# Performance work log

Hardware: AMD Instinct MI355X
Metric: run time of the kernel (lower is better)

## Reference

```python
import math
import jax, jax.numpy as jnp
import numpy as np

K_MODES = 8
L_ITERS = 8
ALPHA_INIT = 2000.0
TAU_INIT = 0.01


def setup_inputs() -> dict:
    key = jax.random.key(0)
    B, T, C = 64, 4096, 16
    x = jax.random.normal(key, (B, T, C), dtype=jnp.float32)
    log_alpha = jnp.full((L_ITERS, K_MODES), math.log(ALPHA_INIT), dtype=jnp.float32)
    raw_tau = jnp.full((L_ITERS,), math.log(math.expm1(TAU_INIT) + 1e-08), dtype=jnp.float32)
    omega_init = np.linspace(0.05, 0.45, K_MODES)
    raw_omega = jnp.asarray(np.log(2.0 * omega_init / (1.0 - 2.0 * omega_init + 1e-08)), dtype=jnp.float32)
    return {"x": x, "log_alpha": log_alpha, "raw_tau": raw_tau, "raw_omega": raw_omega}


def reference(x, log_alpha, raw_tau, raw_omega):
    B, T, C = x.shape
    L, K = log_alpha.shape
    T_rfft = T // 2 + 1

    alpha = jnp.exp(log_alpha)                    # (L, K)
    tau = jax.nn.softplus(raw_tau)                # (L,)
    omega = jax.nn.sigmoid(raw_omega) * 0.5       # (K,)

    freqs = jnp.linspace(0.0, 0.5, T_rfft, dtype=x.dtype)  # (T_rfft,)
    # (B, T, C) -> (B*C, T)
    x_bc = jnp.transpose(x, (0, 2, 1)).reshape(B * C, T)
    f_hat = jnp.fft.rfft(x_bc, axis=-1)           # (B*C, T_rfft) complex

    # Precompute all denominators: (L, K, T_rfft)
    denom = 1.0 + 2.0 * alpha[:, :, None] * (freqs[None, None, :] - omega[None, :, None]) ** 2

    u0 = jnp.zeros((B * C, K, T_rfft), dtype=f_hat.dtype)
    lam0 = jnp.zeros_like(f_hat)

    def step(carry, per_layer):
        u, lam = carry
        den_l, tau_l = per_layer
        u_sum = u.sum(axis=1)  # (B*C, T_rfft)
        # Jacobi update for all K modes simultaneously
        numerator = f_hat[:, None, :] - (u_sum[:, None, :] - u) + 0.5 * lam[:, None, :]
        u_new = numerator / den_l[None, :, :]
        lam_new = lam + tau_l * (f_hat - u_new.sum(axis=1))
        return (u_new, lam_new), None

    (u_final, _), _ = jax.lax.scan(step, (u0, lam0), (denom, tau))

    modes_flat = jnp.fft.irfft(u_final, n=T, axis=-1)  # (B*C, K, T)
    modes = jnp.transpose(modes_flat.reshape(B, C, K, T), (0, 2, 3, 1))  # (B, K, T, C)
    return modes
```

## Files before the change

kernel.cpp:

```cpp
#include <hip/hip_runtime.h>
#include <math.h>

#ifndef M_PI
#define M_PI 3.14159265358979323846
#endif

#define T_LEN 4096
#define M_LEN 2048
#define NFREQ 2049
#define KM 8
#define LI 8
#define CD 16

#define SWZ(i) ((i) ^ (((i) >> 4) & 15))

template <int NT>
__device__ __forceinline__ float2* fft2048(float2* a, float2* b, int tid, float sign) {
    float2* src = a;
    float2* dst = b;
    int l = 1024;
    #pragma unroll 1
    for (int s = 0; s < 11; ++s) {
        float piol = sign * (float)M_PI / (float)l;
        #pragma unroll
        for (int ii = 0; ii < 1024 / NT; ++ii) {
            int i = tid + ii * NT;
            int j = i >> s;
            float2 A = src[i];
            float2 B = src[i + 1024];
            float ang = piol * (float)j;
            float sw, cw;
            __sincosf(ang, &sw, &cw);
            float2 sum = make_float2(A.x + B.x, A.y + B.y);
            float2 dif = make_float2(A.x - B.x, A.y - B.y);
            float2 tw = make_float2(dif.x * cw - dif.y * sw, dif.x * sw + dif.y * cw);
            int p = i + (j << s);
            dst[p] = sum;
            dst[p + (1 << s)] = tw;
        }
        __syncthreads();
        float2* t = src; src = dst; dst = t;
        l >>= 1;
    }
    return src;
}

__global__ void __launch_bounds__(512)
k_fwd_iter(const float* __restrict__ x,
           const float* __restrict__ log_alpha,
           const float* __restrict__ raw_tau,
           const float* __restrict__ raw_omega,
           float2* __restrict__ u_ws)
{
    __shared__ float2 bufA[M_LEN];
    __shared__ float2 bufB[M_LEN];
    __shared__ float s_2a[LI * KM];
    __shared__ float s_tau2[LI];
    __shared__ float s_om[KM];

    const int tid = threadIdx.x;
    const int row = blockIdx.x;
    const int b = row >> 4;
    const int c = row & 15;

    if (tid < LI * KM) s_2a[tid]   = 2.0f * __expf(log_alpha[tid]);
    if (tid < LI)      s_tau2[tid] = 0.5f * log1pf(__expf(raw_tau[tid]));
    if (tid < KM)      s_om[tid]   = 0.5f / (1.0f + __expf(-raw_omega[tid]));

    const float* xr = x + (size_t)b * T_LEN * CD + c;
    #pragma unroll
    for (int q = 0; q < 4; ++q) {
        int n = tid + q * 512;
        float e = xr[(size_t)(2 * n) * CD];
        float o = xr[(size_t)(2 * n + 1) * CD];
        bufA[n] = make_float2(e, o);
    }
    __syncthreads();

    float2* Z = fft2048<512>(bufA, bufB, tid, -1.0f);

    const size_t sb = (size_t)(b * (KM * CD) + c);

    for (int f = tid; f < NFREQ; f += 512) {
        float2 Zk = Z[f & (M_LEN - 1)];
        float2 Zm = Z[(M_LEN - f) & (M_LEN - 1)];
        float2 E = make_float2(0.5f * (Zk.x + Zm.x), 0.5f * (Zk.y - Zm.y));
        float2 D = make_float2(0.5f * (Zk.x - Zm.x), 0.5f * (Zk.y + Zm.y));
        float2 O = make_float2(D.y, -D.x);
        float ang = -2.0f * (float)M_PI * (float)f / (float)T_LEN;
        float sw, cw;
        __sincosf(ang, &sw, &cw);
        float fhx = E.x + cw * O.x - sw * O.y;
        float fhy = E.y + cw * O.y + sw * O.x;

        float freq = (float)f * (0.5f / (float)M_LEN);
        float dd[KM];
        #pragma unroll
        for (int k = 0; k < KM; ++k) {
            float d = freq - s_om[k];
            dd[k] = d * d;
        }

        float2 u[KM];
        float sx, sy;
        float hx, hy;

        {
            float nsx = 0.f, nsy = 0.f;
            #pragma unroll
            for (int k = 0; k < KM; ++k) {
                float den = fmaf(s_2a[k], dd[k], 1.0f);
                float r = __builtin_amdgcn_rcpf(den);
                float ux = fhx * r;
                float uy = fhy * r;
                u[k].x = ux; u[k].y = uy;
                nsx += ux; nsy += uy;
            }
            hx = s_tau2[0] * (fhx - nsx);
            hy = s_tau2[0] * (fhy - nsy);
            sx = nsx; sy = nsy;
        }

        #pragma unroll
        for (int l = 1; l < LI; ++l) {
            float bx = fhx - sx + hx;
            float by = fhy - sy + hy;
            float nsx = 0.f, nsy = 0.f;
            #pragma unroll
            for (int k = 0; k < KM; ++k) {
                float den = fmaf(s_2a[l * KM + k], dd[k], 1.0f);
                float r = __builtin_amdgcn_rcpf(den);
                float ux = (bx + u[k].x) * r;
                float uy = (by + u[k].y) * r;
                u[k].x = ux; u[k].y = uy;
                nsx += ux; nsy += uy;
            }
            hx += s_tau2[l] * (fhx - nsx);
            hy += s_tau2[l] * (fhy - nsy);
            sx = nsx; sy = nsy;
        }

        #pragma unroll
        for (int k = 0; k < KM; ++k) {
            u_ws[(sb + (size_t)k * CD) * NFREQ + f] = u[k];
        }
    }
}

#define R2STAGE(S, SRC, DST, CW, SN) {                                        \
    int j_ = tid >> (S);                                                      \
    float2 A_ = SRC[SWZ(tid)];                                                \
    float2 B_ = SRC[SWZ(tid + 1024)];                                         \
    float2 sum_ = make_float2(A_.x + B_.x, A_.y + B_.y);                      \
    float2 dif_ = make_float2(A_.x - B_.x, A_.y - B_.y);                      \
    float2 tw_ = make_float2(dif_.x * (CW) - dif_.y * (SN),                   \
                             dif_.x * (SN) + dif_.y * (CW));                  \
    int p_ = tid + (j_ << (S));                                               \
    DST[SWZ(p_)] = sum_;                                                      \
    DST[SWZ(p_ + (1 << (S)))] = tw_;                                          \
    __syncthreads();                                                          \
}

#define R2STAGE9(SRC, DST) {                                                  \
    float2 A_ = SRC[SWZ(tid)];                                                \
    float2 B_ = SRC[SWZ(tid + 1024)];                                         \
    float2 sum_ = make_float2(A_.x + B_.x, A_.y + B_.y);                      \
    float2 dif_ = make_float2(A_.x - B_.x, A_.y - B_.y);                      \
    float2 tw_ = (tid & 512) ? make_float2(-dif_.y, dif_.x) : dif_;           \
    int p_ = tid + ((tid >> 9) << 9);                                         \
    DST[SWZ(p_)] = sum_;                                                      \
    DST[SWZ(p_ + 512)] = tw_;                                                 \
    __syncthreads();                                                          \
}

#define R2STAGE10(SRC, DST) {                                                 \
    float2 A_ = SRC[SWZ(tid)];                                                \
    float2 B_ = SRC[SWZ(tid + 1024)];                                         \
    DST[SWZ(tid)] = make_float2(A_.x + B_.x, A_.y + B_.y);                    \
    DST[SWZ(tid + 1024)] = make_float2(A_.x - B_.x, A_.y - B_.y);             \
    __syncthreads();                                                          \
}

__global__ void __launch_bounds__(1024)
k_inv(const float2* __restrict__ u_ws, float* __restrict__ out)
{
    __shared__ float2 bufA[NFREQ];
    __shared__ float2 bufB[M_LEN];
    const int tid = threadIdx.x;
    const int bk = blockIdx.x;

    float cs0,sn0,cs1,sn1,cs2,sn2,cs3,sn3,cs4,sn4,cs5,sn5,cs6,sn6,cs7,sn7,cs8,sn8;
    {
        const float w = (float)M_PI / 1024.0f;
        __sincosf(w * (float)tid,          &sn0, &cs0);
        __sincosf(w * (float)(tid & ~1),   &sn1, &cs1);
        __sincosf(w * (float)(tid & ~3),   &sn2, &cs2);
        __sincosf(w * (float)(tid & ~7),   &sn3, &cs3);
        __sincosf(w * (float)(tid & ~15),  &sn4, &cs4);
        __sincosf(w * (float)(tid & ~31),  &sn5, &cs5);
        __sincosf(w * (float)(tid & ~63),  &sn6, &cs6);
        __sincosf(w * (float)(tid & ~127), &sn7, &cs7);
        __sincosf(w * (float)(tid & ~255), &sn8, &cs8);
    }
    float csR, snR;
    __sincosf(((float)M_PI / 2048.0f) * (float)tid, &snR, &csR);

    float val[CD][4];

    #pragma unroll
    for (int c = 0; c < CD; ++c) {
        const float2* sp = u_ws + (size_t)(bk * CD + c) * NFREQ;
        bufA[SWZ(tid)] = sp[tid];
        bufA[SWZ(tid + 1024)] = sp[tid + 1024];
        if (tid == 0) bufA[2048] = sp[2048];
        __syncthreads();

        const float sc = 1.0f / (float)M_LEN;
        #pragma unroll
        for (int jj = 0; jj < 2; ++jj) {
            int j = tid + jj * 1024;
            float cw = jj ? -snR : csR;
            float sw = jj ?  csR : snR;
            float2 Xj = bufA[SWZ(j)];
            float2 Xm = (j > 0) ? bufA[SWZ(M_LEN - j)] : bufA[2048];
            float2 E = make_float2(0.5f * (Xj.x + Xm.x), 0.5f * (Xj.y - Xm.y));
            float2 D = make_float2(0.5f * (Xj.x - Xm.x), 0.5f * (Xj.y + Xm.y));
            float2 O = make_float2(cw * D.x - sw * D.y, cw * D.y + sw * D.x);
            bufB[SWZ(j)] = make_float2((E.x - O.y) * sc, (E.y + O.x) * sc);
        }
        __syncthreads();

        R2STAGE(0, bufB, bufA, cs0, sn0);
        R2STAGE(1, bufA, bufB, cs1, sn1);
        R2STAGE(2, bufB, bufA, cs2, sn2);
        R2STAGE(3, bufA, bufB, cs3, sn3);
        R2STAGE(4, bufB, bufA, cs4, sn4);
        R2STAGE(5, bufA, bufB, cs5, sn5);
        R2STAGE(6, bufB, bufA, cs6, sn6);
        R2STAGE(7, bufA, bufB, cs7, sn7);
        R2STAGE(8, bufB, bufA, cs8, sn8);
        R2STAGE9(bufA, bufB);
        R2STAGE10(bufB, bufA);

        float2 z0 = bufA[SWZ(2 * tid)];
        float2 z1 = bufA[SWZ(2 * tid + 1)];
        val[c][0] = z0.x;
        val[c][1] = z0.y;
        val[c][2] = z1.x;
        val[c][3] = z1.y;
        __syncthreads();
    }

    float4* op = (float4*)(out + ((size_t)bk * T_LEN + (size_t)(4 * tid)) * CD);
    #pragma unroll
    for (int r = 0; r < 4; ++r) {
        #pragma unroll
        for (int g = 0; g < 4; ++g) {
            op[r * 4 + g] = make_float4(val[4 * g + 0][r], val[4 * g + 1][r],
                                        val[4 * g + 2][r], val[4 * g + 3][r]);
        }
    }
}

extern "C" void kernel_launch(void* const* d_in, const int* in_sizes, int n_in,
                              void* d_out, int out_size, void* d_ws, size_t ws_size,
                              hipStream_t stream) {
    const float* x         = (const float*)d_in[0];
    const float* log_alpha = (const float*)d_in[1];
    const float* raw_tau   = (const float*)d_in[2];
    const float* raw_omega = (const float*)d_in[3];
    float* out = (float*)d_out;
    float2* u_ws = (float2*)d_ws;

    k_fwd_iter<<<dim3(64 * CD), dim3(512), 0, stream>>>(x, log_alpha, raw_tau,
                                                        raw_omega, u_ws);
    k_inv<<<dim3(64 * KM), dim3(1024), 0, stream>>>(u_ws, out);
}
```

Measured before the change: 352.3 us.

## Pack two real channels into one complex 4096-point inverse FFT

Replaces the per-channel half-length real-IFFT (pack, 2048-point complex FFT, post-twiddle) with a two-for-one scheme. Two channels' Hermitian spectra are combined as Xa + i·Xb into a full 4096-point complex spectrum, and one complex IFFT yields both real outputs in the real and imaginary parts. The aim is to halve the number of FFT passes and barriers per channel pair and to drop the separate unpack stage and its shared-memory staging. In exchange each FFT is twice as long, adding one stage and doubling shared-memory use (64 KB), which may cut occupancy.

```diff
diff --git a/kernel.cpp b/kernel.cpp
--- a/kernel.cpp
+++ b/kernel.cpp
@@ -147,107 +147,112 @@
     }
 }
 
-#define R2STAGE(S, SRC, DST, CW, SN) {                                        \
-    int j_ = tid >> (S);                                                      \
-    float2 A_ = SRC[SWZ(tid)];                                                \
-    float2 B_ = SRC[SWZ(tid + 1024)];                                         \
-    float2 sum_ = make_float2(A_.x + B_.x, A_.y + B_.y);                      \
-    float2 dif_ = make_float2(A_.x - B_.x, A_.y - B_.y);                      \
-    float2 tw_ = make_float2(dif_.x * (CW) - dif_.y * (SN),                   \
-                             dif_.x * (SN) + dif_.y * (CW));                  \
-    int p_ = tid + (j_ << (S));                                               \
-    DST[SWZ(p_)] = sum_;                                                      \
-    DST[SWZ(p_ + (1 << (S)))] = tw_;                                          \
+#define R4KSTAGE(S, SRC, DST, CW, SN) {                                       \
+    int j1_ = tid >> (S);                                                     \
+    int p1_ = tid + (j1_ << (S));                                             \
+    int i2_ = tid + 1024;                                                     \
+    int j2_ = i2_ >> (S);                                                     \
+    int p2_ = i2_ + (j2_ << (S));                                             \
+    float2 A1_ = SRC[SWZ(tid)];                                               \
+    float2 B1_ = SRC[SWZ(tid + 2048)];                                        \
+    float2 A2_ = SRC[SWZ(i2_)];                                               \
+    float2 B2_ = SRC[SWZ(i2_ + 2048)];                                        \
+    float2 s1_ = make_float2(A1_.x + B1_.x, A1_.y + B1_.y);                   \
+    float2 d1_ = make_float2(A1_.x - B1_.x, A1_.y - B1_.y);                   \
+    float2 s2_ = make_float2(A2_.x + B2_.x, A2_.y + B2_.y);                   \
+    float2 d2_ = make_float2(A2_.x - B2_.x, A2_.y - B2_.y);                   \
+    DST[SWZ(p1_)] = s1_;                                                      \
+    DST[SWZ(p1_ + (1 << (S)))] =                                              \
+        make_float2(d1_.x * (CW) - d1_.y * (SN),                              \
+                    d1_.x * (SN) + d1_.y * (CW));                             \
+    DST[SWZ(p2_)] = s2_;                                                      \
+    DST[SWZ(p2_ + (1 << (S)))] =                                              \
+        make_float2(-d2_.x * (SN) - d2_.y * (CW),                             \
+                     d2_.x * (CW) - d2_.y * (SN));                            \
     __syncthreads();                                                          \
 }
 
-#define R2STAGE9(SRC, DST) {                                                  \
-    float2 A_ = SRC[SWZ(tid)];                                                \
-    float2 B_ = SRC[SWZ(tid + 1024)];                                         \
-    float2 sum_ = make_float2(A_.x + B_.x, A_.y + B_.y);                      \
-    float2 dif_ = make_float2(A_.x - B_.x, A_.y - B_.y);                      \
-    float2 tw_ = (tid & 512) ? make_float2(-dif_.y, dif_.x) : dif_;           \
-    int p_ = tid + ((tid >> 9) << 9);                                         \
-    DST[SWZ(p_)] = sum_;                                                      \
-    DST[SWZ(p_ + 512)] = tw_;                                                 \
-    __syncthreads();                                                          \
-}
-
-#define R2STAGE10(SRC, DST) {                                                 \
-    float2 A_ = SRC[SWZ(tid)];                                                \
-    float2 B_ = SRC[SWZ(tid + 1024)];                                         \
-    DST[SWZ(tid)] = make_float2(A_.x + B_.x, A_.y + B_.y);                    \
-    DST[SWZ(tid + 1024)] = make_float2(A_.x - B_.x, A_.y - B_.y);             \
+#define R4KSTAGE11(SRC, DST) {                                                \
+    float2 A1_ = SRC[SWZ(tid)];                                               \
+    float2 B1_ = SRC[SWZ(tid + 2048)];                                        \
+    float2 A2_ = SRC[SWZ(tid + 1024)];                                        \
+    float2 B2_ = SRC[SWZ(tid + 3072)];                                        \
+    DST[SWZ(tid)]        = make_float2(A1_.x + B1_.x, A1_.y + B1_.y);         \
+    DST[SWZ(tid + 2048)] = make_float2(A1_.x - B1_.x, A1_.y - B1_.y);         \
+    DST[SWZ(tid + 1024)] = make_float2(A2_.x + B2_.x, A2_.y + B2_.y);         \
+    DST[SWZ(tid + 3072)] = make_float2(A2_.x - B2_.x, A2_.y - B2_.y);         \
     __syncthreads();                                                          \
 }
 
 __global__ void __launch_bounds__(1024)
 k_inv(const float2* __restrict__ u_ws, float* __restrict__ out)
 {
-    __shared__ float2 bufA[NFREQ];
-    __shared__ float2 bufB[M_LEN];
+    __shared__ float2 bufA[2 * M_LEN];
+    __shared__ float2 bufB[2 * M_LEN];
     const int tid = threadIdx.x;
     const int bk = blockIdx.x;
 
-    float cs0,sn0,cs1,sn1,cs2,sn2,cs3,sn3,cs4,sn4,cs5,sn5,cs6,sn6,cs7,sn7,cs8,sn8;
+    float cs0,sn0,cs1,sn1,cs2,sn2,cs3,sn3,cs4,sn4,cs5,sn5,cs6,sn6,cs7,sn7,
+          cs8,sn8,cs9,sn9,cs10,sn10;
     {
-        const float w = (float)M_PI / 1024.0f;
-        __sincosf(w * (float)tid,          &sn0, &cs0);
-        __sincosf(w * (float)(tid & ~1),   &sn1, &cs1);
-        __sincosf(w * (float)(tid & ~3),   &sn2, &cs2);
-        __sincosf(w * (float)(tid & ~7),   &sn3, &cs3);
-        __sincosf(w * (float)(tid & ~15),  &sn4, &cs4);
-        __sincosf(w * (float)(tid & ~31),  &sn5, &cs5);
-        __sincosf(w * (float)(tid & ~63),  &sn6, &cs6);
-        __sincosf(w * (float)(tid & ~127), &sn7, &cs7);
-        __sincosf(w * (float)(tid & ~255), &sn8, &cs8);
-    }
-    float csR, snR;
-    __sincosf(((float)M_PI / 2048.0f) * (float)tid, &snR, &csR);
+        const float w = (float)M_PI / 2048.0f;
+        __sincosf(w * (float)tid,          &sn0,  &cs0);
+        __sincosf(w * (float)(tid & ~1),   &sn1,  &cs1);
+        __sincosf(w * (float)(tid & ~3),   &sn2,  &cs2);
+        __sincosf(w * (float)(tid & ~7),   &sn3,  &cs3);
+        __sincosf(w * (float)(tid & ~15),  &sn4,  &cs4);
+        __sincosf(w * (float)(tid & ~31),  &sn5,  &cs5);
+        __sincosf(w * (float)(tid & ~63),  &sn6,  &cs6);
+        __sincosf(w * (float)(tid & ~127), &sn7,  &cs7);
+        __sincosf(w * (float)(tid & ~255), &sn8,  &cs8);
+        __sincosf(w * (float)(tid & ~511), &sn9,  &cs9);
+        __sincosf(w * (float)(tid & ~1023),&sn10, &cs10);
+    }
 
     float val[CD][4];
+    const float sc = 1.0f / (float)T_LEN;
 
     #pragma unroll
-    for (int c = 0; c < CD; ++c) {
-        const float2* sp = u_ws + (size_t)(bk * CD + c) * NFREQ;
-        bufA[SWZ(tid)] = sp[tid];
-        bufA[SWZ(tid + 1024)] = sp[tid + 1024];
-        if (tid == 0) bufA[2048] = sp[2048];
-        __syncthreads();
-
-        const float sc = 1.0f / (float)M_LEN;
+    for (int cp = 0; cp < 8; ++cp) {
+        const float2* spa = u_ws + (size_t)(bk * CD + 2 * cp) * NFREQ;
+        const float2* spb = spa + NFREQ;
+
         #pragma unroll
         for (int jj = 0; jj < 2; ++jj) {
             int j = tid + jj * 1024;
-            float cw = jj ? -snR : csR;
-            float sw = jj ?  csR : snR;
-            float2 Xj = bufA[SWZ(j)];
-            float2 Xm = (j > 0) ? bufA[SWZ(M_LEN - j)] : bufA[2048];
-            float2 E = make_float2(0.5f * (Xj.x + Xm.x), 0.5f * (Xj.y - Xm.y));
-            float2 D = make_float2(0.5f * (Xj.x - Xm.x), 0.5f * (Xj.y + Xm.y));
-            float2 O = make_float2(cw * D.x - sw * D.y, cw * D.y + sw * D.x);
-            bufB[SWZ(j)] = make_float2((E.x - O.y) * sc, (E.y + O.x) * sc);
+            float2 Xa = spa[j];
+            float2 Xb = spb[j];
+            if (j > 0) {
+                bufA[SWZ(j)]        = make_float2(Xa.x - Xb.y, Xa.y + Xb.x);
+                bufA[SWZ(4096 - j)] = make_float2(Xa.x + Xb.y, Xb.x - Xa.y);
+            } else {
+                bufA[SWZ(0)] = make_float2(Xa.x - Xb.y, Xa.y + Xb.x);
+                float2 Na = spa[2048];
+                float2 Nb = spb[2048];
+                bufA[SWZ(2048)] = make_float2(Na.x - Nb.y, Na.y + Nb.x);
+            }
         }
         __syncthreads();
 
-        R2STAGE(0, bufB, bufA, cs0, sn0);
-        R2STAGE(1, bufA, bufB, cs1, sn1);
-        R2STAGE(2, bufB, bufA, cs2, sn2);
-        R2STAGE(3, bufA, bufB, cs3, sn3);
-        R2STAGE(4, bufB, bufA, cs4, sn4);
-        R2STAGE(5, bufA, bufB, cs5, sn5);
-        R2STAGE(6, bufB, bufA, cs6, sn6);
-        R2STAGE(7, bufA, bufB, cs7, sn7);
-        R2STAGE(8, bufB, bufA, cs8, sn8);
-        R2STAGE9(bufA, bufB);
-        R2STAGE10(bufB, bufA);
-
-        float2 z0 = bufA[SWZ(2 * tid)];
-        float2 z1 = bufA[SWZ(2 * tid + 1)];
-        val[c][0] = z0.x;
-        val[c][1] = z0.y;
-        val[c][2] = z1.x;
-        val[c][3] = z1.y;
+        R4KSTAGE(0,  bufA, bufB, cs0,  sn0);
+        R4KSTAGE(1,  bufB, bufA, cs1,  sn1);
+        R4KSTAGE(2,  bufA, bufB, cs2,  sn2);
+        R4KSTAGE(3,  bufB, bufA, cs3,  sn3);
+        R4KSTAGE(4,  bufA, bufB, cs4,  sn4);
+        R4KSTAGE(5,  bufB, bufA, cs5,  sn5);
+        R4KSTAGE(6,  bufA, bufB, cs6,  sn6);
+        R4KSTAGE(7,  bufB, bufA, cs7,  sn7);
+        R4KSTAGE(8,  bufA, bufB, cs8,  sn8);
+        R4KSTAGE(9,  bufB, bufA, cs9,  sn9);
+        R4KSTAGE(10, bufA, bufB, cs10, sn10);
+        R4KSTAGE11(bufB, bufA);
+
+        #pragma unroll
+        for (int r = 0; r < 4; ++r) {
+            float2 z = bufA[SWZ(4 * tid + r)];
+            val[2 * cp + 0][r] = z.x * sc;
+            val[2 * cp + 1][r] = z.y * sc;
+        }
         __syncthreads();
     }
 
```

Measured after the change: 441.0 us. 1.25x slower.
